# Kernel optimization log

Hardware: AMD Instinct MI355X
Metric: run time of the kernel (lower is better)

Reference implementation:

```python
import jax, jax.numpy as jnp
import numpy as np

N_A = 50000
N_B = 50000
E = 800000
C_IN = 128
C_OUT = 128


def _lstm_cell_seq1(x, W_ih, b):
    # PyTorch LSTM with seq_len=1 and zero initial state: h = o*tanh(i*g)
    # gate order in weight_ih: [i, f, g, o]; f-gate is unused since c0 = 0.
    gates = x @ W_ih.T + b  # [N, 4H]
    i, f, g, o = jnp.split(gates, 4, axis=-1)
    c = jax.nn.sigmoid(i) * jnp.tanh(g)
    return jax.nn.sigmoid(o) * jnp.tanh(c)


def _conv(x_src, x_dst, edge_index, W_ih, b_lstm, W_lin, b_lin):
    # LSTM message depends only on src features -> compute per node, gather per edge.
    msg = _lstm_cell_seq1(x_src, W_ih, b_lstm)          # [N_src, C_OUT]
    src, dst = edge_index[0], edge_index[1]
    aggr = jax.ops.segment_sum(msg[src], dst, num_segments=x_dst.shape[0])  # [N_dst, C_OUT]
    h = jnp.concatenate([x_dst, aggr], axis=-1)          # [N_dst, C_IN + C_OUT]
    return jax.nn.relu(h @ W_lin.T + b_lin)              # dropout = identity (eval mode)


def setup_inputs() -> dict:
    key = jax.random.key(0)
    ks = jax.random.split(key, 12)
    s = 0.05
    return {
        "x_a": jax.random.normal(ks[0], (N_A, C_IN), jnp.float32),
        "x_b": jax.random.normal(ks[1], (N_B, C_IN), jnp.float32),
        "edge_ab": jax.random.randint(ks[2], (2, E), 0, 50000, jnp.int64 if jax.config.jax_enable_x64 else jnp.int32),
        "edge_ba": jax.random.randint(ks[3], (2, E), 0, 50000, jnp.int64 if jax.config.jax_enable_x64 else jnp.int32),
        "W_ih_ab": jax.random.normal(ks[4], (4 * C_OUT, C_IN), jnp.float32) * s,
        "b_ab": jax.random.normal(ks[5], (4 * C_OUT,), jnp.float32) * s,
        "W_lin_ab": jax.random.normal(ks[6], (C_OUT, C_IN + C_OUT), jnp.float32) * s,
        "b_lin_ab": jax.random.normal(ks[7], (C_OUT,), jnp.float32) * s,
        "W_ih_ba": jax.random.normal(ks[8], (4 * C_OUT, C_IN), jnp.float32) * s,
        "b_ba": jax.random.normal(ks[9], (4 * C_OUT,), jnp.float32) * s,
        "W_lin_ba": jax.random.normal(ks[10], (C_OUT, C_IN + C_OUT), jnp.float32) * s,
        "b_lin_ba": jax.random.normal(ks[11], (C_OUT,), jnp.float32) * s,
    }


def reference(x_a, x_b, edge_ab, edge_ba,
              W_ih_ab, b_ab, W_lin_ab, b_lin_ab,
              W_ih_ba, b_ba, W_lin_ba, b_lin_ba):
    # a_to_b relation updates type_b nodes; b_to_a updates type_a nodes.
    out_b = _conv(x_a, x_b, edge_ab, W_ih_ab, b_ab, W_lin_ab, b_lin_ab)
    out_a = _conv(x_b, x_a, edge_ba, W_ih_ba, b_ba, W_lin_ba, b_lin_ba)
    # stack (same shapes) => [2, N, C_OUT]: index 0 = new x_a, index 1 = new x_b
    return jnp.stack([out_a, out_b], axis=0)
```

## Files before the change

### kernel.cpp

```cpp
#include <hip/hip_runtime.h>
#include <cstdint>
#include <cstddef>

#define CCH 128
#define TK 8192
#define FCAP 8192
#define MAXBKT 512
#define XPAD 136
#define APAD 264

typedef __attribute__((ext_vector_type(8))) short short8;
typedef __attribute__((ext_vector_type(4))) float floatx4;

__device__ __forceinline__ unsigned short f2bf(float f) {
    unsigned u = __builtin_bit_cast(unsigned, f);
    u += 0x7fffu + ((u >> 16) & 1u);
    return (unsigned short)(u >> 16);
}
__device__ __forceinline__ float bf2f(unsigned short h) {
    unsigned u = ((unsigned)h) << 16;
    return __builtin_bit_cast(float, u);
}
__device__ __forceinline__ float sigmoidf_(float x) { return 1.0f / (1.0f + __expf(-x)); }

__global__ __launch_bounds__(256) void prep_weights_kernel(
    const float* __restrict__ Wih0, const float* __restrict__ Wih1,
    const float* __restrict__ Wlin0, const float* __restrict__ Wlin1,
    unsigned short* __restrict__ frag_ih, unsigned short* __restrict__ frag_lin)
{
    int t = blockIdx.x * 256 + threadIdx.x;
    if (t < 12288) {
        int l  = t & 63;
        int kc = (t >> 6) & 3;
        int ct = (t >> 8) & 7;
        int g  = (t >> 11) % 3;
        int rel = t / 6144;
        int gb = (g == 0) ? 0 : (g == 1 ? 256 : 384);
        const float* W = rel ? Wih1 : Wih0;
        int n  = gb + ct * 16 + (l & 15);
        int kb = kc * 32 + (l >> 4) * 8;
        unsigned short* o = frag_ih + (size_t)t * 8;
#pragma unroll
        for (int j = 0; j < 8; j++) o[j] = f2bf(W[(size_t)n * CCH + kb + j]);
    } else {
        int t2 = t - 12288;
        if (t2 >= 8192) return;
        int l  = t2 & 63;
        int kc = (t2 >> 6) & 7;
        int ct = (t2 >> 9) & 7;
        int rel = t2 >> 12;
        const float* W = rel ? Wlin1 : Wlin0;
        int n  = ct * 16 + (l & 15);
        int kb = kc * 32 + (l >> 4) * 8;
        unsigned short* o = frag_lin + (size_t)t2 * 8;
#pragma unroll
        for (int j = 0; j < 8; j++) o[j] = f2bf(W[(size_t)n * 256 + kb + j]);
    }
}

__global__ __launch_bounds__(256) void lstm_hist_kernel(
    const float* __restrict__ x0, const float* __restrict__ x1,
    const unsigned short* __restrict__ wfrag,
    const float* __restrict__ b0, const float* __restrict__ b1,
    unsigned short* __restrict__ msg0, unsigned short* __restrict__ msg1,
    int N0, int N1, int nblk0,
    const int* __restrict__ dstE0, const int* __restrict__ dstE1,
    int* __restrict__ H, int E0, int E1, int nbkt0, int NBKT, int nT)
{
    __shared__ unsigned short xs[32 * XPAD];
    __shared__ int h[MAXBKT];
    const int tid = threadIdx.x;

    if (blockIdx.x < nT) {
        for (int i = tid; i < NBKT; i += 256) h[i] = 0;
        __syncthreads();
        const long long Etot = (long long)E0 + E1;
        const long long base = (long long)blockIdx.x * TK;
        for (int i = tid; i < TK; i += 256) {
            long long e = base + i;
            if (e >= Etot) break;
            int g;
            if (e < E0) g = dstE0[e] >> 8;
            else        g = nbkt0 + (dstE1[e - E0] >> 8);
            atomicAdd(&h[g], 1);
        }
        __syncthreads();
        int* row = H + (size_t)blockIdx.x * NBKT;
        for (int i = tid; i < NBKT; i += 256) row[i] = h[i];
        return;
    }

    const int lb = blockIdx.x - nT;
    const int rel = (lb >= nblk0);
    const int nb = (rel ? (lb - nblk0) : lb) * 32;
    const float* x = rel ? x1 : x0;
    const float* bias = rel ? b1 : b0;
    unsigned short* msg = rel ? msg1 : msg0;
    const int N = rel ? N1 : N0;
    const unsigned short* wf = wfrag + (size_t)rel * 6144 * 8;

    {
        int r = tid >> 3;
        int c0 = (tid & 7) * 16;
        int n = nb + r;
        unsigned short* dstp = xs + r * XPAD + c0;
        if (n < N) {
            const float4* srcp = (const float4*)(x + (size_t)n * CCH + c0);
#pragma unroll
            for (int qq = 0; qq < 4; qq++) {
                float4 v = srcp[qq];
                unsigned u0 = (unsigned)f2bf(v.x) | ((unsigned)f2bf(v.y) << 16);
                unsigned u1 = (unsigned)f2bf(v.z) | ((unsigned)f2bf(v.w) << 16);
                *(uint2*)(dstp + qq * 4) = make_uint2(u0, u1);
            }
        } else {
#pragma unroll
            for (int qq = 0; qq < 4; qq++) *(uint2*)(dstp + qq * 4) = make_uint2(0u, 0u);
        }
    }
    __syncthreads();

    const int w = tid >> 6;
    const int l = tid & 63;
    const int ctb2 = w * 2;
    const int q = l >> 4;
    const int m16 = l & 15;

    floatx4 acc[3][2][2];
#pragma unroll
    for (int g = 0; g < 3; g++)
#pragma unroll
        for (int c = 0; c < 2; c++)
#pragma unroll
            for (int mt = 0; mt < 2; mt++) acc[g][c][mt] = (floatx4){0.f, 0.f, 0.f, 0.f};

    const unsigned short* arow0 = xs + m16 * XPAD + q * 8;
    const unsigned short* arow1 = xs + (16 + m16) * XPAD + q * 8;
#pragma unroll
    for (int kc = 0; kc < 4; kc++) {
        short8 af0 = *(const short8*)(arow0 + kc * 32);
        short8 af1 = *(const short8*)(arow1 + kc * 32);
#pragma unroll
        for (int g = 0; g < 3; g++)
#pragma unroll
            for (int c = 0; c < 2; c++) {
                const unsigned short* bp = wf + ((((size_t)g * 8 + (ctb2 + c)) * 4 + kc) * 64 + l) * 8;
                short8 bv = *(const short8*)bp;
                acc[g][c][0] = __builtin_amdgcn_mfma_f32_16x16x32_bf16(af0, bv, acc[g][c][0], 0, 0, 0);
                acc[g][c][1] = __builtin_amdgcn_mfma_f32_16x16x32_bf16(af1, bv, acc[g][c][1], 0, 0, 0);
            }
    }

#pragma unroll
    for (int c = 0; c < 2; c++) {
        const int col = (ctb2 + c) * 16 + m16;
        const float bi = bias[col], bg = bias[256 + col], bo = bias[384 + col];
#pragma unroll
        for (int mt = 0; mt < 2; mt++)
#pragma unroll
            for (int r = 0; r < 4; r++) {
                const int node = nb + mt * 16 + q * 4 + r;
                if (node < N) {
                    float iv = sigmoidf_(acc[0][c][mt][r] + bi);
                    float gv = tanhf(acc[1][c][mt][r] + bg);
                    float ov = sigmoidf_(acc[2][c][mt][r] + bo);
                    msg[(size_t)node * CCH + col] = f2bf(ov * tanhf(iv * gv));
                }
            }
    }
}

__global__ __launch_bounds__(256) void colscan_kernel(
    int* __restrict__ H, int* __restrict__ btot, int nT, int NBKT)
{
    __shared__ int s[256];
    __shared__ int carry;
    const int g = blockIdx.x;
    const int tid = threadIdx.x;
    if (tid == 0) carry = 0;
    __syncthreads();
    for (int base = 0; base < nT; base += 256) {
        int b = base + tid;
        int v = (b < nT) ? H[(size_t)b * NBKT + g] : 0;
        s[tid] = v;
        __syncthreads();
#pragma unroll
        for (int off = 1; off < 256; off <<= 1) {
            int t = (tid >= off) ? s[tid - off] : 0;
            __syncthreads();
            s[tid] += t;
            __syncthreads();
        }
        if (b < nT) H[(size_t)b * NBKT + g] = s[tid] - v + carry;
        __syncthreads();
        if (tid == 255) carry += s[255];
        __syncthreads();
    }
    if (tid == 0) btot[g] = carry;
}

__global__ __launch_bounds__(256) void scanb_kernel(
    const int* __restrict__ btot, int* __restrict__ coff, int NBKT)
{
    __shared__ int s[256];
    __shared__ int carry;
    const int tid = threadIdx.x;
    if (tid == 0) carry = 0;
    __syncthreads();
    for (int base = 0; base < NBKT; base += 256) {
        int i = base + tid;
        int v = (i < NBKT) ? btot[i] : 0;
        s[tid] = v;
        __syncthreads();
#pragma unroll
        for (int off = 1; off < 256; off <<= 1) {
            int t = (tid >= off) ? s[tid - off] : 0;
            __syncthreads();
            s[tid] += t;
            __syncthreads();
        }
        if (i < NBKT) coff[i] = s[tid] - v + carry;
        __syncthreads();
        if (tid == 255) carry += s[255];
        __syncthreads();
    }
}

__global__ __launch_bounds__(256) void tile_scatter_kernel(
    const int* __restrict__ src0, const int* __restrict__ dst0,
    const int* __restrict__ src1, const int* __restrict__ dst1,
    const int* __restrict__ H, const int* __restrict__ coff,
    unsigned* __restrict__ packed, int E0, int E1, int nbkt0, int NBKT)
{
    __shared__ int cur[MAXBKT];
    const int tid = threadIdx.x;
    const int* row = H + (size_t)blockIdx.x * NBKT;
    for (int i = tid; i < NBKT; i += 256) cur[i] = coff[i] + row[i];
    __syncthreads();
    const long long Etot = (long long)E0 + E1;
    const long long base = (long long)blockIdx.x * TK;
    for (int i = tid; i < TK; i += 256) {
        long long e = base + i;
        if (e >= Etot) break;
        int s, g, k;
        if (e < E0) { int d = dst0[e]; s = src0[e]; g = d >> 8; k = d & 255; }
        else { long long ee = e - E0; int d = dst1[ee]; s = src1[ee]; g = nbkt0 + (d >> 8); k = d & 255; }
        int pos = atomicAdd(&cur[g], 1);
        packed[pos] = ((unsigned)k << 24) | (unsigned)s;
    }
}

__global__ __launch_bounds__(256) void fine_sort_kernel(
    unsigned* __restrict__ packed, const int* __restrict__ coff, const int* __restrict__ btot,
    int* __restrict__ offs0, int* __restrict__ deg0,
    int* __restrict__ offs1, int* __restrict__ deg1,
    int N0, int N1, int nbkt0)
{
    __shared__ unsigned pin[FCAP];
    __shared__ int sout[FCAP];
    __shared__ int hist[256], scn[256], cur[256];
    const int g = blockIdx.x;
    const int tid = threadIdx.x;
    const int base = coff[g];
    const int cnt = min(btot[g], FCAP);

    for (int i = tid; i < cnt; i += 256) pin[i] = packed[base + i];
    hist[tid] = 0;
    __syncthreads();
    for (int i = tid; i < cnt; i += 256) atomicAdd(&hist[pin[i] >> 24], 1);
    __syncthreads();
    int v = hist[tid];
    scn[tid] = v;
    __syncthreads();
#pragma unroll
    for (int off = 1; off < 256; off <<= 1) {
        int t = (tid >= off) ? scn[tid - off] : 0;
        __syncthreads();
        scn[tid] += t;
        __syncthreads();
    }
    int excl = scn[tid] - v;
    cur[tid] = excl;
    {
        const int rel = (g >= nbkt0);
        const int lb = rel ? g - nbkt0 : g;
        const int n = lb * 256 + tid;
        const int N = rel ? N1 : N0;
        if (n < N) {
            if (rel) { offs1[n] = base + excl; deg1[n] = v; }
            else     { offs0[n] = base + excl; deg0[n] = v; }
        }
    }
    __syncthreads();
    for (int i = tid; i < cnt; i += 256) {
        unsigned p = pin[i];
        int pos = atomicAdd(&cur[p >> 24], 1);
        sout[pos] = (int)(p & 0x00FFFFFFu);
    }
    __syncthreads();
    int* op = (int*)packed;
    for (int i = tid; i < cnt; i += 256) op[base + i] = sout[i];
}

__global__ __launch_bounds__(256) void gather_kernel(
    const unsigned short* __restrict__ msg0, const unsigned short* __restrict__ msg1,
    const int* __restrict__ csr,
    const int* __restrict__ offs0, const int* __restrict__ offs1,
    const int* __restrict__ deg0, const int* __restrict__ deg1,
    unsigned short* __restrict__ aggr0, unsigned short* __restrict__ aggr1,
    int N0, int N1)
{
    const int wv = blockIdx.x * 4 + (threadIdx.x >> 6);
    const int l = threadIdx.x & 63;
    const unsigned short* msg; unsigned short* aggr;
    int n, start, cnt;
    if (wv < N0)            { n = wv;      msg = msg0; start = offs0[n]; cnt = deg0[n]; aggr = aggr0; }
    else if (wv < N0 + N1)  { n = wv - N0; msg = msg1; start = offs1[n]; cnt = deg1[n]; aggr = aggr1; }
    else return;

    float ax = 0.f, ay = 0.f;
    const int* ce = csr + start;
    const unsigned short* mb = msg + l * 2;
    int j = 0;
    for (; j + 8 <= cnt; j += 8) {
        int s0 = ce[j], s1 = ce[j + 1], s2 = ce[j + 2], s3 = ce[j + 3];
        int s4 = ce[j + 4], s5 = ce[j + 5], s6 = ce[j + 6], s7 = ce[j + 7];
        unsigned u0 = *(const unsigned*)(mb + (size_t)s0 * CCH);
        unsigned u1 = *(const unsigned*)(mb + (size_t)s1 * CCH);
        unsigned u2 = *(const unsigned*)(mb + (size_t)s2 * CCH);
        unsigned u3 = *(const unsigned*)(mb + (size_t)s3 * CCH);
        unsigned u4 = *(const unsigned*)(mb + (size_t)s4 * CCH);
        unsigned u5 = *(const unsigned*)(mb + (size_t)s5 * CCH);
        unsigned u6 = *(const unsigned*)(mb + (size_t)s6 * CCH);
        unsigned u7 = *(const unsigned*)(mb + (size_t)s7 * CCH);
        ax += bf2f((unsigned short)u0) + bf2f((unsigned short)u1)
            + bf2f((unsigned short)u2) + bf2f((unsigned short)u3)
            + bf2f((unsigned short)u4) + bf2f((unsigned short)u5)
            + bf2f((unsigned short)u6) + bf2f((unsigned short)u7);
        ay += bf2f((unsigned short)(u0 >> 16)) + bf2f((unsigned short)(u1 >> 16))
            + bf2f((unsigned short)(u2 >> 16)) + bf2f((unsigned short)(u3 >> 16))
            + bf2f((unsigned short)(u4 >> 16)) + bf2f((unsigned short)(u5 >> 16))
            + bf2f((unsigned short)(u6 >> 16)) + bf2f((unsigned short)(u7 >> 16));
    }
    for (; j + 4 <= cnt; j += 4) {
        int s0 = ce[j], s1 = ce[j + 1], s2 = ce[j + 2], s3 = ce[j + 3];
        unsigned u0 = *(const unsigned*)(mb + (size_t)s0 * CCH);
        unsigned u1 = *(const unsigned*)(mb + (size_t)s1 * CCH);
        unsigned u2 = *(const unsigned*)(mb + (size_t)s2 * CCH);
        unsigned u3 = *(const unsigned*)(mb + (size_t)s3 * CCH);
        ax += bf2f((unsigned short)u0) + bf2f((unsigned short)u1)
            + bf2f((unsigned short)u2) + bf2f((unsigned short)u3);
        ay += bf2f((unsigned short)(u0 >> 16)) + bf2f((unsigned short)(u1 >> 16))
            + bf2f((unsigned short)(u2 >> 16)) + bf2f((unsigned short)(u3 >> 16));
    }
    for (; j < cnt; j++) {
        unsigned u0 = *(const unsigned*)(mb + (size_t)ce[j] * CCH);
        ax += bf2f((unsigned short)u0);
        ay += bf2f((unsigned short)(u0 >> 16));
    }
    unsigned o = (unsigned)f2bf(ax) | ((unsigned)f2bf(ay) << 16);
    *(unsigned*)(aggr + (size_t)n * CCH + l * 2) = o;
}

__global__ __launch_bounds__(256) void linear_mfma_kernel(
    const float* __restrict__ xd0, const float* __restrict__ xd1,
    const unsigned short* __restrict__ ag0, const unsigned short* __restrict__ ag1,
    const unsigned short* __restrict__ wfrag,
    const float* __restrict__ bl0, const float* __restrict__ bl1,
    float* __restrict__ out0, float* __restrict__ out1,
    int N0, int N1, int nblk0)
{
    __shared__ unsigned short s[32 * APAD];
    const int rel = (blockIdx.x >= nblk0);
    const int nb = (rel ? blockIdx.x - nblk0 : blockIdx.x) * 32;
    const float* xd = rel ? xd1 : xd0;
    const unsigned short* ag = rel ? ag1 : ag0;
    const float* bl = rel ? bl1 : bl0;
    float* outp = rel ? out1 : out0;
    const int N = rel ? N1 : N0;
    const unsigned short* wf = wfrag + (size_t)rel * 4096 * 8;

    {
        int t = threadIdx.x;
        int r = t >> 3;
        int c0 = (t & 7) * 16;
        int n = nb + r;
        unsigned short* drow = s + r * APAD;
        if (n < N) {
            const float4* srcp = (const float4*)(xd + (size_t)n * CCH + c0);
#pragma unroll
            for (int qq = 0; qq < 4; qq++) {
                float4 v = srcp[qq];
                unsigned u0 = (unsigned)f2bf(v.x) | ((unsigned)f2bf(v.y) << 16);
                unsigned u1 = (unsigned)f2bf(v.z) | ((unsigned)f2bf(v.w) << 16);
                *(uint2*)(drow + c0 + qq * 4) = make_uint2(u0, u1);
            }
            const uint4* ap = (const uint4*)(ag + (size_t)n * CCH + c0);
            *(uint4*)(drow + CCH + c0) = ap[0];
            *(uint4*)(drow + CCH + c0 + 8) = ap[1];
        } else {
            uint4 z = make_uint4(0u, 0u, 0u, 0u);
            *(uint4*)(drow + c0) = z;
            *(uint4*)(drow + c0 + 8) = z;
            *(uint4*)(drow + CCH + c0) = z;
            *(uint4*)(drow + CCH + c0 + 8) = z;
        }
    }
    __syncthreads();

    const int tid = threadIdx.x;
    const int w = tid >> 6;
    const int l = tid & 63;
    const int ctb2 = w * 2;
    const int q = l >> 4;
    const int m16 = l & 15;

    floatx4 acc[2][2];
#pragma unroll
    for (int c = 0; c < 2; c++)
#pragma unroll
        for (int mt = 0; mt < 2; mt++) acc[c][mt] = (floatx4){0.f, 0.f, 0.f, 0.f};

    const unsigned short* arow0 = s + m16 * APAD + q * 8;
    const unsigned short* arow1 = s + (16 + m16) * APAD + q * 8;
#pragma unroll
    for (int kc = 0; kc < 8; kc++) {
        short8 af0 = *(const short8*)(arow0 + kc * 32);
        short8 af1 = *(const short8*)(arow1 + kc * 32);
#pragma unroll
        for (int c = 0; c < 2; c++) {
            const unsigned short* bp = wf + ((((size_t)(ctb2 + c)) * 8 + kc) * 64 + l) * 8;
            short8 bv = *(const short8*)bp;
            acc[c][0] = __builtin_amdgcn_mfma_f32_16x16x32_bf16(af0, bv, acc[c][0], 0, 0, 0);
            acc[c][1] = __builtin_amdgcn_mfma_f32_16x16x32_bf16(af1, bv, acc[c][1], 0, 0, 0);
        }
    }

#pragma unroll
    for (int c = 0; c < 2; c++) {
        const int col = (ctb2 + c) * 16 + m16;
        const float bv = bl[col];
#pragma unroll
        for (int mt = 0; mt < 2; mt++)
#pragma unroll
            for (int r = 0; r < 4; r++) {
                const int node = nb + mt * 16 + q * 4 + r;
                if (node < N) outp[(size_t)node * CCH + col] = fmaxf(acc[c][mt][r] + bv, 0.0f);
            }
    }
}

extern "C" void kernel_launch(void* const* d_in, const int* in_sizes, int n_in,
                              void* d_out, int out_size, void* d_ws, size_t ws_size,
                              hipStream_t stream) {
    const float* x_a      = (const float*)d_in[0];
    const float* x_b      = (const float*)d_in[1];
    const int*   e_ab     = (const int*)d_in[2];
    const int*   e_ba     = (const int*)d_in[3];
    const float* W_ih_ab  = (const float*)d_in[4];
    const float* b_ab     = (const float*)d_in[5];
    const float* W_lin_ab = (const float*)d_in[6];
    const float* b_lin_ab = (const float*)d_in[7];
    const float* W_ih_ba  = (const float*)d_in[8];
    const float* b_ba     = (const float*)d_in[9];
    const float* W_lin_ba = (const float*)d_in[10];
    const float* b_lin_ba = (const float*)d_in[11];

    const int NA = in_sizes[0] / CCH;
    const int NB = in_sizes[1] / CCH;
    const int E0 = in_sizes[2] / 2;
    const int E1 = in_sizes[3] / 2;

    float* out = (float*)d_out;
    char* ws = (char*)d_ws;
    size_t off = 0;
    auto alloc = [&](size_t bytes) { char* p = ws + off; off += (bytes + 255) & ~(size_t)255; return p; };

    unsigned short* wfrag_ih  = (unsigned short*)alloc(12288 * 8 * 2);
    unsigned short* wfrag_lin = (unsigned short*)alloc(8192 * 8 * 2);
    unsigned short* msg_a     = (unsigned short*)alloc((size_t)NA * CCH * 2);
    unsigned short* msg_b     = (unsigned short*)alloc((size_t)NB * CCH * 2);
    unsigned short* aggr_b    = (unsigned short*)alloc((size_t)NB * CCH * 2);
    unsigned short* aggr_a    = (unsigned short*)alloc((size_t)NA * CCH * 2);

    const int nbkt0 = (NB + 255) / 256;
    const int nbkt1 = (NA + 255) / 256;
    const int NBKT = nbkt0 + nbkt1;
    const long long Etot = (long long)E0 + E1;
    const int nT = (int)((Etot + TK - 1) / TK);

    int* H      = (int*)alloc((size_t)nT * NBKT * 4);
    int* btot   = (int*)alloc((size_t)NBKT * 4);
    int* coff   = (int*)alloc((size_t)NBKT * 4);
    int* offs_b = (int*)alloc((size_t)NB * 4);
    int* offs_a = (int*)alloc((size_t)NA * 4);
    int* deg_b  = (int*)alloc((size_t)NB * 4);
    int* deg_a  = (int*)alloc((size_t)NA * 4);
    unsigned* packed = (unsigned*)alloc((size_t)Etot * 4);

    const int nblkA = (NA + 31) / 32;
    const int nblkB = (NB + 31) / 32;

    prep_weights_kernel<<<80, 256, 0, stream>>>(
        W_ih_ab, W_ih_ba, W_lin_ab, W_lin_ba, wfrag_ih, wfrag_lin);

    lstm_hist_kernel<<<nT + nblkA + nblkB, 256, 0, stream>>>(
        x_a, x_b, wfrag_ih, b_ab, b_ba, msg_a, msg_b, NA, NB, nblkA,
        e_ab + E0, e_ba + E1, H, E0, E1, nbkt0, NBKT, nT);

    colscan_kernel<<<NBKT, 256, 0, stream>>>(H, btot, nT, NBKT);
    scanb_kernel<<<1, 256, 0, stream>>>(btot, coff, NBKT);
    tile_scatter_kernel<<<nT, 256, 0, stream>>>(
        e_ab, e_ab + E0, e_ba, e_ba + E1, H, coff, packed, E0, E1, nbkt0, NBKT);
    fine_sort_kernel<<<NBKT, 256, 0, stream>>>(
        packed, coff, btot, offs_b, deg_b, offs_a, deg_a, NB, NA, nbkt0);

    gather_kernel<<<(NB + NA + 3) / 4, 256, 0, stream>>>(
        msg_a, msg_b, (const int*)packed, offs_b, offs_a, deg_b, deg_a, aggr_b, aggr_a, NB, NA);

    linear_mfma_kernel<<<nblkB + nblkA, 256, 0, stream>>>(
        x_b, x_a, aggr_b, aggr_a, wfrag_lin, b_lin_ab, b_lin_ba,
        out + (size_t)NA * CCH, out, NB, NA, nblkB);
}
```

Measured before the change: 286.6 us.

## Fuse gather into linear MFMA kernel, use fixed bucket slots, fast tanh

Merges the per-node neighbor gather with the output linear layer so aggregated messages go straight into shared memory instead of round-tripping through global aggr buffers. Drops the bucket-offset scan kernel by giving each coarse bucket a fixed SLOT-sized region. It also replaces tanhf with a clamped exp-based tanh in the LSTM epilogue. In exchange the fixed slots silently truncate any bucket holding more than 8192 edges, and each linear block now does its own irregular gather work. The 512-thread blocks also use one MFMA column tile per wave.

```diff
diff --git a/kernel.cpp b/kernel.cpp
--- a/kernel.cpp
+++ b/kernel.cpp
@@ -5,6 +5,7 @@
 #define CCH 128
 #define TK 8192
 #define FCAP 8192
+#define SLOT 8192
 #define MAXBKT 512
 #define XPAD 136
 #define APAD 264
@@ -22,6 +23,11 @@
     return __builtin_bit_cast(float, u);
 }
 __device__ __forceinline__ float sigmoidf_(float x) { return 1.0f / (1.0f + __expf(-x)); }
+__device__ __forceinline__ float tanh_fast(float x) {
+    x = fminf(fmaxf(x, -10.0f), 10.0f);
+    float e = __expf(2.0f * x);
+    return (e - 1.0f) / (e + 1.0f);
+}
 
 __global__ __launch_bounds__(256) void prep_weights_kernel(
     const float* __restrict__ Wih0, const float* __restrict__ Wih1,
@@ -162,9 +168,9 @@
                 const int node = nb + mt * 16 + q * 4 + r;
                 if (node < N) {
                     float iv = sigmoidf_(acc[0][c][mt][r] + bi);
-                    float gv = tanhf(acc[1][c][mt][r] + bg);
+                    float gv = tanh_fast(acc[1][c][mt][r] + bg);
                     float ov = sigmoidf_(acc[2][c][mt][r] + bo);
-                    msg[(size_t)node * CCH + col] = f2bf(ov * tanhf(iv * gv));
+                    msg[(size_t)node * CCH + col] = f2bf(ov * tanh_fast(iv * gv));
                 }
             }
     }
@@ -199,43 +205,16 @@
     if (tid == 0) btot[g] = carry;
 }
 
-__global__ __launch_bounds__(256) void scanb_kernel(
-    const int* __restrict__ btot, int* __restrict__ coff, int NBKT)
-{
-    __shared__ int s[256];
-    __shared__ int carry;
-    const int tid = threadIdx.x;
-    if (tid == 0) carry = 0;
-    __syncthreads();
-    for (int base = 0; base < NBKT; base += 256) {
-        int i = base + tid;
-        int v = (i < NBKT) ? btot[i] : 0;
-        s[tid] = v;
-        __syncthreads();
-#pragma unroll
-        for (int off = 1; off < 256; off <<= 1) {
-            int t = (tid >= off) ? s[tid - off] : 0;
-            __syncthreads();
-            s[tid] += t;
-            __syncthreads();
-        }
-        if (i < NBKT) coff[i] = s[tid] - v + carry;
-        __syncthreads();
-        if (tid == 255) carry += s[255];
-        __syncthreads();
-    }
-}
-
 __global__ __launch_bounds__(256) void tile_scatter_kernel(
     const int* __restrict__ src0, const int* __restrict__ dst0,
     const int* __restrict__ src1, const int* __restrict__ dst1,
-    const int* __restrict__ H, const int* __restrict__ coff,
+    const int* __restrict__ H,
     unsigned* __restrict__ packed, int E0, int E1, int nbkt0, int NBKT)
 {
     __shared__ int cur[MAXBKT];
     const int tid = threadIdx.x;
     const int* row = H + (size_t)blockIdx.x * NBKT;
-    for (int i = tid; i < NBKT; i += 256) cur[i] = coff[i] + row[i];
+    for (int i = tid; i < NBKT; i += 256) cur[i] = i * SLOT + row[i];
     __syncthreads();
     const long long Etot = (long long)E0 + E1;
     const long long base = (long long)blockIdx.x * TK;
@@ -251,7 +230,7 @@
 }
 
 __global__ __launch_bounds__(256) void fine_sort_kernel(
-    unsigned* __restrict__ packed, const int* __restrict__ coff, const int* __restrict__ btot,
+    unsigned* __restrict__ packed, const int* __restrict__ btot,
     int* __restrict__ offs0, int* __restrict__ deg0,
     int* __restrict__ offs1, int* __restrict__ deg1,
     int N0, int N1, int nbkt0)
@@ -261,7 +240,7 @@
     __shared__ int hist[256], scn[256], cur[256];
     const int g = blockIdx.x;
     const int tid = threadIdx.x;
-    const int base = coff[g];
+    const int base = g * SLOT;
     const int cnt = min(btot[g], FCAP);
 
     for (int i = tid; i < cnt; i += 256) pin[i] = packed[base + i];
@@ -302,124 +281,118 @@
     for (int i = tid; i < cnt; i += 256) op[base + i] = sout[i];
 }
 
-__global__ __launch_bounds__(256) void gather_kernel(
+__global__ __launch_bounds__(512) void gather_linear_kernel(
+    const float* __restrict__ xd0, const float* __restrict__ xd1,
     const unsigned short* __restrict__ msg0, const unsigned short* __restrict__ msg1,
     const int* __restrict__ csr,
     const int* __restrict__ offs0, const int* __restrict__ offs1,
     const int* __restrict__ deg0, const int* __restrict__ deg1,
-    unsigned short* __restrict__ aggr0, unsigned short* __restrict__ aggr1,
-    int N0, int N1)
-{
-    const int wv = blockIdx.x * 4 + (threadIdx.x >> 6);
-    const int l = threadIdx.x & 63;
-    const unsigned short* msg; unsigned short* aggr;
-    int n, start, cnt;
-    if (wv < N0)            { n = wv;      msg = msg0; start = offs0[n]; cnt = deg0[n]; aggr = aggr0; }
-    else if (wv < N0 + N1)  { n = wv - N0; msg = msg1; start = offs1[n]; cnt = deg1[n]; aggr = aggr1; }
-    else return;
-
-    float ax = 0.f, ay = 0.f;
-    const int* ce = csr + start;
-    const unsigned short* mb = msg + l * 2;
-    int j = 0;
-    for (; j + 8 <= cnt; j += 8) {
-        int s0 = ce[j], s1 = ce[j + 1], s2 = ce[j + 2], s3 = ce[j + 3];
-        int s4 = ce[j + 4], s5 = ce[j + 5], s6 = ce[j + 6], s7 = ce[j + 7];
-        unsigned u0 = *(const unsigned*)(mb + (size_t)s0 * CCH);
-        unsigned u1 = *(const unsigned*)(mb + (size_t)s1 * CCH);
-        unsigned u2 = *(const unsigned*)(mb + (size_t)s2 * CCH);
-        unsigned u3 = *(const unsigned*)(mb + (size_t)s3 * CCH);
-        unsigned u4 = *(const unsigned*)(mb + (size_t)s4 * CCH);
-        unsigned u5 = *(const unsigned*)(mb + (size_t)s5 * CCH);
-        unsigned u6 = *(const unsigned*)(mb + (size_t)s6 * CCH);
-        unsigned u7 = *(const unsigned*)(mb + (size_t)s7 * CCH);
-        ax += bf2f((unsigned short)u0) + bf2f((unsigned short)u1)
-            + bf2f((unsigned short)u2) + bf2f((unsigned short)u3)
-            + bf2f((unsigned short)u4) + bf2f((unsigned short)u5)
-            + bf2f((unsigned short)u6) + bf2f((unsigned short)u7);
-        ay += bf2f((unsigned short)(u0 >> 16)) + bf2f((unsigned short)(u1 >> 16))
-            + bf2f((unsigned short)(u2 >> 16)) + bf2f((unsigned short)(u3 >> 16))
-            + bf2f((unsigned short)(u4 >> 16)) + bf2f((unsigned short)(u5 >> 16))
-            + bf2f((unsigned short)(u6 >> 16)) + bf2f((unsigned short)(u7 >> 16));
-    }
-    for (; j + 4 <= cnt; j += 4) {
-        int s0 = ce[j], s1 = ce[j + 1], s2 = ce[j + 2], s3 = ce[j + 3];
-        unsigned u0 = *(const unsigned*)(mb + (size_t)s0 * CCH);
-        unsigned u1 = *(const unsigned*)(mb + (size_t)s1 * CCH);
-        unsigned u2 = *(const unsigned*)(mb + (size_t)s2 * CCH);
-        unsigned u3 = *(const unsigned*)(mb + (size_t)s3 * CCH);
-        ax += bf2f((unsigned short)u0) + bf2f((unsigned short)u1)
-            + bf2f((unsigned short)u2) + bf2f((unsigned short)u3);
-        ay += bf2f((unsigned short)(u0 >> 16)) + bf2f((unsigned short)(u1 >> 16))
-            + bf2f((unsigned short)(u2 >> 16)) + bf2f((unsigned short)(u3 >> 16));
-    }
-    for (; j < cnt; j++) {
-        unsigned u0 = *(const unsigned*)(mb + (size_t)ce[j] * CCH);
-        ax += bf2f((unsigned short)u0);
-        ay += bf2f((unsigned short)(u0 >> 16));
-    }
-    unsigned o = (unsigned)f2bf(ax) | ((unsigned)f2bf(ay) << 16);
-    *(unsigned*)(aggr + (size_t)n * CCH + l * 2) = o;
-}
-
-__global__ __launch_bounds__(256) void linear_mfma_kernel(
-    const float* __restrict__ xd0, const float* __restrict__ xd1,
-    const unsigned short* __restrict__ ag0, const unsigned short* __restrict__ ag1,
     const unsigned short* __restrict__ wfrag,
     const float* __restrict__ bl0, const float* __restrict__ bl1,
     float* __restrict__ out0, float* __restrict__ out1,
-    int N0, int N1, int nblk0)
+    int P0, int P1, int N0, int N1)
 {
     __shared__ unsigned short s[32 * APAD];
-    const int rel = (blockIdx.x >= nblk0);
-    const int nb = (rel ? blockIdx.x - nblk0 : blockIdx.x) * 32;
+    const int tid = threadIdx.x;
+    const int grp = blockIdx.x >> 3;
+    const int sub = blockIdx.x & 7;
+    const int rel = (sub >> 2) & 1;
+    const int lb = grp * 4 + (sub & 3);
+    const int P = rel ? P1 : P0;
+    if (lb >= P) return;
+    const int nb = lb * 32;
     const float* xd = rel ? xd1 : xd0;
-    const unsigned short* ag = rel ? ag1 : ag0;
+    const unsigned short* msg = rel ? msg1 : msg0;
+    const int* offs = rel ? offs1 : offs0;
+    const int* deg = rel ? deg1 : deg0;
     const float* bl = rel ? bl1 : bl0;
     float* outp = rel ? out1 : out0;
     const int N = rel ? N1 : N0;
     const unsigned short* wf = wfrag + (size_t)rel * 4096 * 8;
 
     {
-        int t = threadIdx.x;
-        int r = t >> 3;
-        int c0 = (t & 7) * 16;
+        int r = tid >> 4;
+        int c0 = (tid & 15) * 8;
         int n = nb + r;
-        unsigned short* drow = s + r * APAD;
+        unsigned short* drow = s + r * APAD + c0;
         if (n < N) {
             const float4* srcp = (const float4*)(xd + (size_t)n * CCH + c0);
-#pragma unroll
-            for (int qq = 0; qq < 4; qq++) {
-                float4 v = srcp[qq];
-                unsigned u0 = (unsigned)f2bf(v.x) | ((unsigned)f2bf(v.y) << 16);
-                unsigned u1 = (unsigned)f2bf(v.z) | ((unsigned)f2bf(v.w) << 16);
-                *(uint2*)(drow + c0 + qq * 4) = make_uint2(u0, u1);
+            float4 v0 = srcp[0], v1 = srcp[1];
+            uint4 u;
+            u.x = (unsigned)f2bf(v0.x) | ((unsigned)f2bf(v0.y) << 16);
+            u.y = (unsigned)f2bf(v0.z) | ((unsigned)f2bf(v0.w) << 16);
+            u.z = (unsigned)f2bf(v1.x) | ((unsigned)f2bf(v1.y) << 16);
+            u.w = (unsigned)f2bf(v1.z) | ((unsigned)f2bf(v1.w) << 16);
+            *(uint4*)drow = u;
+        } else {
+            *(uint4*)drow = make_uint4(0u, 0u, 0u, 0u);
+        }
+    }
+    {
+        const int w = tid >> 6;
+        const int l = tid & 63;
+        const unsigned short* mb = msg + l * 2;
+#pragma unroll
+        for (int m = 0; m < 4; m++) {
+            const int nloc = w * 4 + m;
+            const int n = nb + nloc;
+            float ax = 0.f, ay = 0.f;
+            if (n < N) {
+                const int start = offs[n];
+                const int cnt = deg[n];
+                const int* ce = csr + start;
+                int j = 0;
+                for (; j + 8 <= cnt; j += 8) {
+                    int s0 = ce[j], s1 = ce[j + 1], s2 = ce[j + 2], s3 = ce[j + 3];
+                    int s4 = ce[j + 4], s5 = ce[j + 5], s6 = ce[j + 6], s7 = ce[j + 7];
+                    unsigned u0 = *(const unsigned*)(mb + (size_t)s0 * CCH);
+                    unsigned u1 = *(const unsigned*)(mb + (size_t)s1 * CCH);
+                    unsigned u2 = *(const unsigned*)(mb + (size_t)s2 * CCH);
+                    unsigned u3 = *(const unsigned*)(mb + (size_t)s3 * CCH);
+                    unsigned u4 = *(const unsigned*)(mb + (size_t)s4 * CCH);
+                    unsigned u5 = *(const unsigned*)(mb + (size_t)s5 * CCH);
+                    unsigned u6 = *(const unsigned*)(mb + (size_t)s6 * CCH);
+                    unsigned u7 = *(const unsigned*)(mb + (size_t)s7 * CCH);
+                    ax += bf2f((unsigned short)u0) + bf2f((unsigned short)u1)
+                        + bf2f((unsigned short)u2) + bf2f((unsigned short)u3)
+                        + bf2f((unsigned short)u4) + bf2f((unsigned short)u5)
+                        + bf2f((unsigned short)u6) + bf2f((unsigned short)u7);
+                    ay += bf2f((unsigned short)(u0 >> 16)) + bf2f((unsigned short)(u1 >> 16))
+                        + bf2f((unsigned short)(u2 >> 16)) + bf2f((unsigned short)(u3 >> 16))
+                        + bf2f((unsigned short)(u4 >> 16)) + bf2f((unsigned short)(u5 >> 16))
+                        + bf2f((unsigned short)(u6 >> 16)) + bf2f((unsigned short)(u7 >> 16));
+                }
+                for (; j + 4 <= cnt; j += 4) {
+                    int s0 = ce[j], s1 = ce[j + 1], s2 = ce[j + 2], s3 = ce[j + 3];
+                    unsigned u0 = *(const unsigned*)(mb + (size_t)s0 * CCH);
+                    unsigned u1 = *(const unsigned*)(mb + (size_t)s1 * CCH);
+                    unsigned u2 = *(const unsigned*)(mb + (size_t)s2 * CCH);
+                    unsigned u3 = *(const unsigned*)(mb + (size_t)s3 * CCH);
+                    ax += bf2f((unsigned short)u0) + bf2f((unsigned short)u1)
+                        + bf2f((unsigned short)u2) + bf2f((unsigned short)u3);
+                    ay += bf2f((unsigned short)(u0 >> 16)) + bf2f((unsigned short)(u1 >> 16))
+                        + bf2f((unsigned short)(u2 >> 16)) + bf2f((unsigned short)(u3 >> 16));
+                }
+                for (; j < cnt; j++) {
+                    unsigned u0 = *(const unsigned*)(mb + (size_t)ce[j] * CCH);
+                    ax += bf2f((unsigned short)u0);
+                    ay += bf2f((unsigned short)(u0 >> 16));
+                }
             }
-            const uint4* ap = (const uint4*)(ag + (size_t)n * CCH + c0);
-            *(uint4*)(drow + CCH + c0) = ap[0];
-            *(uint4*)(drow + CCH + c0 + 8) = ap[1];
-        } else {
-            uint4 z = make_uint4(0u, 0u, 0u, 0u);
-            *(uint4*)(drow + c0) = z;
-            *(uint4*)(drow + c0 + 8) = z;
-            *(uint4*)(drow + CCH + c0) = z;
-            *(uint4*)(drow + CCH + c0 + 8) = z;
-        }
-    }
-    __syncthreads();
-
-    const int tid = threadIdx.x;
+            unsigned o = (unsigned)f2bf(ax) | ((unsigned)f2bf(ay) << 16);
+            *(unsigned*)(s + nloc * APAD + CCH + l * 2) = o;
+        }
+    }
+    __syncthreads();
+
     const int w = tid >> 6;
     const int l = tid & 63;
-    const int ctb2 = w * 2;
     const int q = l >> 4;
     const int m16 = l & 15;
 
-    floatx4 acc[2][2];
-#pragma unroll
-    for (int c = 0; c < 2; c++)
-#pragma unroll
-        for (int mt = 0; mt < 2; mt++) acc[c][mt] = (floatx4){0.f, 0.f, 0.f, 0.f};
+    floatx4 acc[2];
+    acc[0] = (floatx4){0.f, 0.f, 0.f, 0.f};
+    acc[1] = (floatx4){0.f, 0.f, 0.f, 0.f};
 
     const unsigned short* arow0 = s + m16 * APAD + q * 8;
     const unsigned short* arow1 = s + (16 + m16) * APAD + q * 8;
@@ -427,27 +400,21 @@
     for (int kc = 0; kc < 8; kc++) {
         short8 af0 = *(const short8*)(arow0 + kc * 32);
         short8 af1 = *(const short8*)(arow1 + kc * 32);
-#pragma unroll
-        for (int c = 0; c < 2; c++) {
-            const unsigned short* bp = wf + ((((size_t)(ctb2 + c)) * 8 + kc) * 64 + l) * 8;
-            short8 bv = *(const short8*)bp;
-            acc[c][0] = __builtin_amdgcn_mfma_f32_16x16x32_bf16(af0, bv, acc[c][0], 0, 0, 0);
-            acc[c][1] = __builtin_amdgcn_mfma_f32_16x16x32_bf16(af1, bv, acc[c][1], 0, 0, 0);
-        }
-    }
-
-#pragma unroll
-    for (int c = 0; c < 2; c++) {
-        const int col = (ctb2 + c) * 16 + m16;
-        const float bv = bl[col];
-#pragma unroll
-        for (int mt = 0; mt < 2; mt++)
-#pragma unroll
-            for (int r = 0; r < 4; r++) {
-                const int node = nb + mt * 16 + q * 4 + r;
-                if (node < N) outp[(size_t)node * CCH + col] = fmaxf(acc[c][mt][r] + bv, 0.0f);
-            }
-    }
+        const unsigned short* bp = wf + ((((size_t)w) * 8 + kc) * 64 + l) * 8;
+        short8 bv = *(const short8*)bp;
+        acc[0] = __builtin_amdgcn_mfma_f32_16x16x32_bf16(af0, bv, acc[0], 0, 0, 0);
+        acc[1] = __builtin_amdgcn_mfma_f32_16x16x32_bf16(af1, bv, acc[1], 0, 0, 0);
+    }
+
+    const int col = w * 16 + m16;
+    const float bv = bl[col];
+#pragma unroll
+    for (int mt = 0; mt < 2; mt++)
+#pragma unroll
+        for (int r = 0; r < 4; r++) {
+            const int node = nb + mt * 16 + q * 4 + r;
+            if (node < N) outp[(size_t)node * CCH + col] = fmaxf(acc[mt][r] + bv, 0.0f);
+        }
 }
 
 extern "C" void kernel_launch(void* const* d_in, const int* in_sizes, int n_in,
@@ -480,8 +447,6 @@
     unsigned short* wfrag_lin = (unsigned short*)alloc(8192 * 8 * 2);
     unsigned short* msg_a     = (unsigned short*)alloc((size_t)NA * CCH * 2);
     unsigned short* msg_b     = (unsigned short*)alloc((size_t)NB * CCH * 2);
-    unsigned short* aggr_b    = (unsigned short*)alloc((size_t)NB * CCH * 2);
-    unsigned short* aggr_a    = (unsigned short*)alloc((size_t)NA * CCH * 2);
 
     const int nbkt0 = (NB + 255) / 256;
     const int nbkt1 = (NA + 255) / 256;
@@ -491,12 +456,11 @@
 
     int* H      = (int*)alloc((size_t)nT * NBKT * 4);
     int* btot   = (int*)alloc((size_t)NBKT * 4);
-    int* coff   = (int*)alloc((size_t)NBKT * 4);
     int* offs_b = (int*)alloc((size_t)NB * 4);
     int* offs_a = (int*)alloc((size_t)NA * 4);
     int* deg_b  = (int*)alloc((size_t)NB * 4);
     int* deg_a  = (int*)alloc((size_t)NA * 4);
-    unsigned* packed = (unsigned*)alloc((size_t)Etot * 4);
+    unsigned* packed = (unsigned*)alloc((size_t)NBKT * SLOT * 4);
 
     const int nblkA = (NA + 31) / 32;
     const int nblkB = (NB + 31) / 32;
@@ -509,16 +473,15 @@
         e_ab + E0, e_ba + E1, H, E0, E1, nbkt0, NBKT, nT);
 
     colscan_kernel<<<NBKT, 256, 0, stream>>>(H, btot, nT, NBKT);
-    scanb_kernel<<<1, 256, 0, stream>>>(btot, coff, NBKT);
     tile_scatter_kernel<<<nT, 256, 0, stream>>>(
-        e_ab, e_ab + E0, e_ba, e_ba + E1, H, coff, packed, E0, E1, nbkt0, NBKT);
+        e_ab, e_ab + E0, e_ba, e_ba + E1, H, packed, E0, E1, nbkt0, NBKT);
     fine_sort_kernel<<<NBKT, 256, 0, stream>>>(
-        packed, coff, btot, offs_b, deg_b, offs_a, deg_a, NB, NA, nbkt0);
-
-    gather_kernel<<<(NB + NA + 3) / 4, 256, 0, stream>>>(
-        msg_a, msg_b, (const int*)packed, offs_b, offs_a, deg_b, deg_a, aggr_b, aggr_a, NB, NA);
-
-    linear_mfma_kernel<<<nblkB + nblkA, 256, 0, stream>>>(
-        x_b, x_a, aggr_b, aggr_a, wfrag_lin, b_lin_ab, b_lin_ba,
-        out + (size_t)NA * CCH, out, NB, NA, nblkB);
-}
+        packed, btot, offs_b, deg_b, offs_a, deg_a, NB, NA, nbkt0);
+
+    const int Pmax = (nblkB > nblkA) ? nblkB : nblkA;
+    const int G = ((Pmax + 3) / 4) * 8;
+    gather_linear_kernel<<<G, 512, 0, stream>>>(
+        x_b, x_a, msg_a, msg_b, (const int*)packed,
+        offs_b, offs_a, deg_b, deg_a, wfrag_lin, b_lin_ab, b_lin_ba,
+        out + (size_t)NA * CCH, out, nblkB, nblkA, NB, NA);
+}
```

Measured after the change: 279.8 us. 2.4% less time.
